# Optimization experiments

Hardware: AMD Instinct MI355X
Metric: run time of the kernel (lower is better)

## Reference

```python
import jax, jax.numpy as jnp
import numpy as np

N_NODES = 50000
N_EDGES = 800000
D = 64
H = 128


def setup_inputs() -> dict:
    key = jax.random.key(0)
    ks = jax.random.split(key, 8)
    s = 0.05
    return {
        "nodes": jax.random.normal(ks[0], (N_NODES, D), jnp.float32),
        "edges": jax.random.normal(ks[1], (N_EDGES, D), jnp.float32),
        "We1": jax.random.normal(ks[2], (3 * D, H), jnp.float32) * s,
        "be1": jnp.zeros((H,), jnp.float32),
        "We2": jax.random.normal(ks[3], (H, D), jnp.float32) * s,
        "be2": jnp.zeros((D,), jnp.float32),
        "Wn1": jax.random.normal(ks[4], (2 * D, H), jnp.float32) * s,
        "bn1": jnp.zeros((H,), jnp.float32),
        "Wn2": jax.random.normal(ks[5], (H, D), jnp.float32) * s,
        "bn2": jnp.zeros((D,), jnp.float32),
        "senders": jax.random.randint(ks[6], (N_EDGES,), 0, N_NODES, jnp.int32),
        "receivers": jax.random.randint(ks[7], (N_EDGES,), 0, N_NODES, jnp.int32),
    }


def reference(nodes, edges, We1, be1, We2, be2, Wn1, bn1, Wn2, bn2, senders, receivers):
    # EdgeBlock(use_globals=False): concat[edge, receiver_node, sender_node] -> MLP
    edge_in = jnp.concatenate([edges, nodes[receivers], nodes[senders]], axis=-1)  # [E, 3D]
    h = jax.nn.relu(edge_in @ We1 + be1)
    new_edges = h @ We2 + be2  # [E, D]

    # NodeBlock(use_sent_edges=False, use_globals=False):
    # aggregate received edges via segment_sum, concat with node feats -> MLP
    agg = jax.ops.segment_sum(new_edges, receivers, num_segments=nodes.shape[0])  # [N, D]
    node_in = jnp.concatenate([agg, nodes], axis=-1)  # [N, 2D]
    h2 = jax.nn.relu(node_in @ Wn1 + bn1)
    new_nodes = h2 @ Wn2 + bn2  # [N, D]
    return new_nodes
```

## Files before the change

kernel.cpp:

```cpp
#include <hip/hip_runtime.h>

#define NN 50000
#define NE 800000

typedef __attribute__((ext_vector_type(8))) short bf16x8;
typedef __attribute__((ext_vector_type(8))) unsigned short us8;
typedef __attribute__((ext_vector_type(4))) unsigned short us4;
typedef __attribute__((ext_vector_type(4))) float f32x4;

#define MFMA16 __builtin_amdgcn_mfma_f32_16x16x32_bf16

__device__ __forceinline__ unsigned short f2b(float f) {
    union { float f; unsigned int u; } x; x.f = f;
    unsigned int r = x.u + 0x7FFFu + ((x.u >> 16) & 1u);
    return (unsigned short)(r >> 16);
}

__device__ __forceinline__ void atomic_pk_add_bf16(unsigned short* addr, unsigned int pk) {
    asm volatile("global_atomic_pk_add_bf16 %0, %1, off" :: "v"(addr), "v"(pk) : "memory");
}

__global__ __launch_bounds__(256) void prep_kernel(
    const float* __restrict__ nodes,
    const float* __restrict__ We1, const float* __restrict__ We2,
    const float* __restrict__ Wn1, const float* __restrict__ Wn2,
    unsigned short* __restrict__ nodes_bf,
    unsigned short* __restrict__ We1T, unsigned short* __restrict__ We2T,
    unsigned short* __restrict__ Wn1T, unsigned short* __restrict__ Wn2T)
{
    const int b = blockIdx.x, t = threadIdx.x;
    if (b < 400) {
        const float4* src = (const float4*)nodes;
        for (int i = b * 256 + t; i < NN * 16; i += 400 * 256) {
            float4 v = src[i];
            us4 o; o[0] = f2b(v.x); o[1] = f2b(v.y); o[2] = f2b(v.z); o[3] = f2b(v.w);
            *(us4*)&nodes_bf[(size_t)i * 4] = o;
        }
    } else {
        const int base = (b - 400) * 256 + t;
        for (int idx = base; idx < 57344; idx += 16 * 256) {
            if (idx < 24576) {
                int n = idx / 192, k = idx % 192;
                We1T[idx] = f2b(We1[k * 128 + n]);
            } else if (idx < 32768) {
                int j = idx - 24576; int n = j / 128, k = j % 128;
                We2T[j] = f2b(We2[k * 64 + n]);
            } else if (idx < 49152) {
                int j = idx - 32768; int n = j / 128, k = j % 128;
                Wn1T[j] = f2b(Wn1[k * 128 + n]);
            } else {
                int j = idx - 49152; int n = j / 128, k = j % 128;
                Wn2T[j] = f2b(Wn2[k * 64 + n]);
            }
        }
    }
}

__global__ __launch_bounds__(256, 6) void edge_kernel(
    const unsigned short* __restrict__ nodes_bf, const float* __restrict__ edges,
    const unsigned short* __restrict__ We1T, const float* __restrict__ be1,
    const unsigned short* __restrict__ We2T, const float* __restrict__ be2,
    const int* __restrict__ senders, const int* __restrict__ receivers,
    unsigned short* __restrict__ agg_bf)
{
    __shared__ __align__(16) unsigned short xs[64 * 200];
    __shared__ int ridx[64];
    __shared__ int sidx[64];

    const int t = threadIdx.x;
    const int e0 = blockIdx.x * 64;
    const int w = t >> 6, l = t & 63, lc = l & 15, lq = l >> 4;

    if (t < 64) {
        ridx[t] = receivers[e0 + t];
        sidx[t] = senders[e0 + t];
    }

    bf16x8 wA0[6], wA1[6], wB[4];
    #pragma unroll
    for (int c = 0; c < 6; ++c) {
        wA0[c] = *(const bf16x8*)&We1T[(w * 32 + lc) * 192 + c * 32 + lq * 8];
        wA1[c] = *(const bf16x8*)&We1T[(w * 32 + 16 + lc) * 192 + c * 32 + lq * 8];
    }
    #pragma unroll
    for (int c = 0; c < 4; ++c)
        wB[c] = *(const bf16x8*)&We2T[(w * 16 + lc) * 128 + c * 32 + lq * 8];
    const float b1x = be1[w * 32 + lc];
    const float b1y = be1[w * 32 + 16 + lc];
    const float bias2 = be2[w * 16 + lc];

    __syncthreads();

    #pragma unroll
    for (int i = 0; i < 4; ++i) {
        int idx = t + 256 * i;
        int m = idx >> 4, q = idx & 15;
        float4 v = *(const float4*)&edges[((size_t)(e0 + m)) * 64 + q * 4];
        us4 o; o[0] = f2b(v.x); o[1] = f2b(v.y); o[2] = f2b(v.z); o[3] = f2b(v.w);
        *(us4*)&xs[m * 200 + q * 4] = o;
    }
    #pragma unroll
    for (int i = 0; i < 2; ++i) {
        int idx = t + 256 * i;
        int m = idx >> 3, q = idx & 7;
        us8 v = *(const us8*)&nodes_bf[(size_t)ridx[m] * 64 + q * 8];
        *(us8*)&xs[m * 200 + 64 + q * 8] = v;
    }
    #pragma unroll
    for (int i = 0; i < 2; ++i) {
        int idx = t + 256 * i;
        int m = idx >> 3, q = idx & 7;
        us8 v = *(const us8*)&nodes_bf[(size_t)sidx[m] * 64 + q * 8];
        *(us8*)&xs[m * 200 + 128 + q * 8] = v;
    }
    __syncthreads();

    f32x4 acc[4][2];
    #pragma unroll
    for (int mt = 0; mt < 4; ++mt) { acc[mt][0] = (f32x4)0.f; acc[mt][1] = (f32x4)0.f; }
    #pragma unroll
    for (int c = 0; c < 6; ++c) {
        #pragma unroll
        for (int mt = 0; mt < 4; ++mt) {
            bf16x8 a = *(const bf16x8*)&xs[(mt * 16 + lc) * 200 + c * 32 + lq * 8];
            acc[mt][0] = MFMA16(a, wA0[c], acc[mt][0], 0, 0, 0);
            acc[mt][1] = MFMA16(a, wA1[c], acc[mt][1], 0, 0, 0);
        }
    }
    __syncthreads();

    #pragma unroll
    for (int nt = 0; nt < 2; ++nt) {
        int col = w * 32 + nt * 16 + lc;
        float bias = nt ? b1y : b1x;
        #pragma unroll
        for (int mt = 0; mt < 4; ++mt) {
            #pragma unroll
            for (int r = 0; r < 4; ++r) {
                int row = mt * 16 + lq * 4 + r;
                float v = fmaxf(acc[mt][nt][r] + bias, 0.f);
                xs[row * 136 + col] = f2b(v);
            }
        }
    }
    __syncthreads();

    f32x4 acc2[4];
    #pragma unroll
    for (int mt = 0; mt < 4; ++mt) acc2[mt] = (f32x4)0.f;
    #pragma unroll
    for (int c = 0; c < 4; ++c) {
        #pragma unroll
        for (int mt = 0; mt < 4; ++mt) {
            bf16x8 a = *(const bf16x8*)&xs[(mt * 16 + lc) * 136 + c * 32 + lq * 8];
            acc2[mt] = MFMA16(a, wB[c], acc2[mt], 0, 0, 0);
        }
    }
    __syncthreads();

    float* fs = (float*)xs;
    {
        const int col = w * 16 + lc;
        #pragma unroll
        for (int mt = 0; mt < 4; ++mt) {
            #pragma unroll
            for (int r = 0; r < 4; ++r) {
                int row = mt * 16 + lq * 4 + r;
                fs[row * 68 + col] = acc2[mt][r] + bias2;
            }
        }
    }
    __syncthreads();

    #pragma unroll
    for (int i = 0; i < 8; ++i) {
        int p = t + 256 * i;
        int row = p >> 5, cp = p & 31;
        float2 v = *(const float2*)&fs[row * 68 + cp * 2];
        unsigned int pk = (unsigned int)f2b(v.x) | ((unsigned int)f2b(v.y) << 16);
        atomic_pk_add_bf16(&agg_bf[(size_t)ridx[row] * 64 + cp * 2], pk);
    }
}

__global__ __launch_bounds__(256, 6) void node_kernel(
    const unsigned short* __restrict__ nodes_bf, const unsigned short* __restrict__ agg_bf,
    const unsigned short* __restrict__ Wn1T, const float* __restrict__ bn1,
    const unsigned short* __restrict__ Wn2T, const float* __restrict__ bn2,
    float* __restrict__ out)
{
    __shared__ __align__(16) unsigned short xs[64 * 136];

    const int t = threadIdx.x;
    const int n0 = blockIdx.x * 64;
    const int w = t >> 6, l = t & 63, lc = l & 15, lq = l >> 4;

    bf16x8 wA0[4], wA1[4], wB[4];
    #pragma unroll
    for (int c = 0; c < 4; ++c) {
        wA0[c] = *(const bf16x8*)&Wn1T[(w * 32 + lc) * 128 + c * 32 + lq * 8];
        wA1[c] = *(const bf16x8*)&Wn1T[(w * 32 + 16 + lc) * 128 + c * 32 + lq * 8];
        wB[c]  = *(const bf16x8*)&Wn2T[(w * 16 + lc) * 128 + c * 32 + lq * 8];
    }
    const float b1x = bn1[w * 32 + lc];
    const float b1y = bn1[w * 32 + 16 + lc];
    const float bias2 = bn2[w * 16 + lc];

    #pragma unroll
    for (int i = 0; i < 2; ++i) {
        int idx = t + 256 * i;
        int m = idx >> 3, q = idx & 7;
        int n = n0 + m;
        us8 v = {0, 0, 0, 0, 0, 0, 0, 0};
        if (n < NN) v = *(const us8*)&agg_bf[(size_t)n * 64 + q * 8];
        *(us8*)&xs[m * 136 + q * 8] = v;
    }
    #pragma unroll
    for (int i = 0; i < 2; ++i) {
        int idx = t + 256 * i;
        int m = idx >> 3, q = idx & 7;
        int n = n0 + m;
        us8 v = {0, 0, 0, 0, 0, 0, 0, 0};
        if (n < NN) v = *(const us8*)&nodes_bf[(size_t)n * 64 + q * 8];
        *(us8*)&xs[m * 136 + 64 + q * 8] = v;
    }
    __syncthreads();

    f32x4 acc[4][2];
    #pragma unroll
    for (int mt = 0; mt < 4; ++mt) { acc[mt][0] = (f32x4)0.f; acc[mt][1] = (f32x4)0.f; }
    #pragma unroll
    for (int c = 0; c < 4; ++c) {
        #pragma unroll
        for (int mt = 0; mt < 4; ++mt) {
            bf16x8 a = *(const bf16x8*)&xs[(mt * 16 + lc) * 136 + c * 32 + lq * 8];
            acc[mt][0] = MFMA16(a, wA0[c], acc[mt][0], 0, 0, 0);
            acc[mt][1] = MFMA16(a, wA1[c], acc[mt][1], 0, 0, 0);
        }
    }
    __syncthreads();

    #pragma unroll
    for (int nt = 0; nt < 2; ++nt) {
        int col = w * 32 + nt * 16 + lc;
        float bias = nt ? b1y : b1x;
        #pragma unroll
        for (int mt = 0; mt < 4; ++mt) {
            #pragma unroll
            for (int r = 0; r < 4; ++r) {
                int row = mt * 16 + lq * 4 + r;
                float v = fmaxf(acc[mt][nt][r] + bias, 0.f);
                xs[row * 136 + col] = f2b(v);
            }
        }
    }
    __syncthreads();

    f32x4 acc2[4];
    #pragma unroll
    for (int mt = 0; mt < 4; ++mt) acc2[mt] = (f32x4)0.f;
    #pragma unroll
    for (int c = 0; c < 4; ++c) {
        #pragma unroll
        for (int mt = 0; mt < 4; ++mt) {
            bf16x8 a = *(const bf16x8*)&xs[(mt * 16 + lc) * 136 + c * 32 + lq * 8];
            acc2[mt] = MFMA16(a, wB[c], acc2[mt], 0, 0, 0);
        }
    }

    const int col = w * 16 + lc;
    #pragma unroll
    for (int mt = 0; mt < 4; ++mt) {
        #pragma unroll
        for (int r = 0; r < 4; ++r) {
            int row = mt * 16 + lq * 4 + r;
            int n = n0 + row;
            if (n < NN) out[(size_t)n * 64 + col] = acc2[mt][r] + bias2;
        }
    }
}

extern "C" void kernel_launch(void* const* d_in, const int* in_sizes, int n_in,
                              void* d_out, int out_size, void* d_ws, size_t ws_size,
                              hipStream_t stream) {
    const float* nodes = (const float*)d_in[0];
    const float* edges = (const float*)d_in[1];
    const float* We1   = (const float*)d_in[2];
    const float* be1   = (const float*)d_in[3];
    const float* We2   = (const float*)d_in[4];
    const float* be2   = (const float*)d_in[5];
    const float* Wn1   = (const float*)d_in[6];
    const float* bn1   = (const float*)d_in[7];
    const float* Wn2   = (const float*)d_in[8];
    const float* bn2   = (const float*)d_in[9];
    const int* senders   = (const int*)d_in[10];
    const int* receivers = (const int*)d_in[11];
    float* out = (float*)d_out;

    char* ws = (char*)d_ws;
    unsigned short* agg_bf = (unsigned short*)ws;
    unsigned short* nodes_bf = (unsigned short*)(ws + 12800000);
    unsigned short* We1T = (unsigned short*)(ws + 19200000);
    unsigned short* We2T = (unsigned short*)(ws + 19249152);
    unsigned short* Wn1T = (unsigned short*)(ws + 19265536);
    unsigned short* Wn2T = (unsigned short*)(ws + 19298304);

    hipMemsetAsync(agg_bf, 0, (size_t)NN * 64 * sizeof(unsigned short), stream);
    prep_kernel<<<416, 256, 0, stream>>>(nodes, We1, We2, Wn1, Wn2,
                                         nodes_bf, We1T, We2T, Wn1T, Wn2T);
    edge_kernel<<<NE / 64, 256, 0, stream>>>(nodes_bf, edges, We1T, be1, We2T, be2,
                                             senders, receivers, agg_bf);
    node_kernel<<<(NN + 63) / 64, 256, 0, stream>>>(nodes_bf, agg_bf, Wn1T, bn1, Wn2T, bn2, out);
}
```

Before: 508.4 us.

## Sort edges by receiver and reduce runs in-block before scattering to aggregates

Adds a counting-sort pipeline (histogram, three-stage scan, permutation) that groups edges by receiver. The edge kernel then processes edges in sorted order and sums each run of equal receivers in shared memory. It issues one atomic per run, or a plain store when the run is wholly inside the block. The goal is to cut the atomic traffic of the bf16 scatter. The cost is several extra small kernels and memsets, plus an indirect gather of edge rows through the permutation, which loses coalescing. Occupancy hints for edge_kernel and node_kernel are lowered from 6 to 4.

```diff
diff --git a/kernel.cpp b/kernel.cpp
--- a/kernel.cpp
+++ b/kernel.cpp
@@ -2,6 +2,8 @@
 
 #define NN 50000
 #define NE 800000
+#define NNP 50176
+#define SCANB 196
 
 typedef __attribute__((ext_vector_type(8))) short bf16x8;
 typedef __attribute__((ext_vector_type(8))) unsigned short us8;
@@ -56,24 +58,103 @@
     }
 }
 
-__global__ __launch_bounds__(256, 6) void edge_kernel(
+__global__ __launch_bounds__(256) void hist_kernel(
+    const int* __restrict__ receivers, int* __restrict__ deg)
+{
+    int e = blockIdx.x * 256 + threadIdx.x;
+    if (e < NE) atomicAdd(&deg[receivers[e]], 1);
+}
+
+__global__ __launch_bounds__(256) void scan1_kernel(
+    const int* __restrict__ deg, int* __restrict__ psum)
+{
+    __shared__ int red[256];
+    int t = threadIdx.x;
+    red[t] = deg[blockIdx.x * 256 + t];
+    __syncthreads();
+    for (int s = 128; s > 0; s >>= 1) {
+        if (t < s) red[t] += red[t + s];
+        __syncthreads();
+    }
+    if (t == 0) psum[blockIdx.x] = red[0];
+}
+
+__global__ __launch_bounds__(256) void scan2_kernel(
+    const int* __restrict__ psum, int* __restrict__ poff)
+{
+    __shared__ int a[256];
+    int t = threadIdx.x;
+    int v0 = (t < SCANB) ? psum[t] : 0;
+    a[t] = v0;
+    __syncthreads();
+    for (int off = 1; off < 256; off <<= 1) {
+        int x = a[t];
+        if (t >= off) x += a[t - off];
+        __syncthreads();
+        a[t] = x;
+        __syncthreads();
+    }
+    poff[t] = a[t] - v0;
+}
+
+__global__ __launch_bounds__(256) void scan3_kernel(
+    const int* __restrict__ deg, const int* __restrict__ poff, int* __restrict__ basep)
+{
+    __shared__ int a[256];
+    int t = threadIdx.x, i = blockIdx.x * 256 + t;
+    int v0 = deg[i];
+    a[t] = v0;
+    __syncthreads();
+    for (int off = 1; off < 256; off <<= 1) {
+        int x = a[t];
+        if (t >= off) x += a[t - off];
+        __syncthreads();
+        a[t] = x;
+        __syncthreads();
+    }
+    basep[i] = poff[blockIdx.x] + a[t] - v0;
+}
+
+__global__ __launch_bounds__(256) void perm_kernel(
+    const int* __restrict__ receivers, const int* __restrict__ senders,
+    const int* __restrict__ basep, int* __restrict__ cursor,
+    int* __restrict__ perm, int* __restrict__ rsorted, int* __restrict__ ssorted)
+{
+    int e = blockIdx.x * 256 + threadIdx.x;
+    if (e < NE) {
+        int r = receivers[e];
+        int pos = basep[r] + atomicAdd(&cursor[r], 1);
+        perm[pos] = e;
+        rsorted[pos] = r;
+        ssorted[pos] = senders[e];
+    }
+}
+
+__global__ __launch_bounds__(256, 4) void edge_kernel(
     const unsigned short* __restrict__ nodes_bf, const float* __restrict__ edges,
     const unsigned short* __restrict__ We1T, const float* __restrict__ be1,
     const unsigned short* __restrict__ We2T, const float* __restrict__ be2,
-    const int* __restrict__ senders, const int* __restrict__ receivers,
+    const int* __restrict__ perm, const int* __restrict__ rsorted,
+    const int* __restrict__ ssorted, const int* __restrict__ basep,
     unsigned short* __restrict__ agg_bf)
 {
     __shared__ __align__(16) unsigned short xs[64 * 200];
+    __shared__ int eidx[64];
     __shared__ int ridx[64];
     __shared__ int sidx[64];
+    __shared__ int runStart[65];
+    __shared__ int runRecv[64];
+    __shared__ int runFull[64];
+    __shared__ int nrunsS;
 
     const int t = threadIdx.x;
     const int e0 = blockIdx.x * 64;
     const int w = t >> 6, l = t & 63, lc = l & 15, lq = l >> 4;
 
     if (t < 64) {
-        ridx[t] = receivers[e0 + t];
-        sidx[t] = senders[e0 + t];
+        eidx[t] = perm[e0 + t];
+        ridx[t] = rsorted[e0 + t];
+        sidx[t] = ssorted[e0 + t];
     }
 
     bf16x8 wA0[6], wA1[6], wB[4];
@@ -91,11 +172,26 @@
 
     __syncthreads();
 
+    if (t < 64) {
+        int n = ridx[t];
+        bool flag = (t == 0) || (n != ridx[t - 1]);
+        unsigned long long mask = __ballot(flag);
+        int nr = __popcll(mask);
+        if (t == 0) { nrunsS = nr; runStart[nr] = 64; }
+        if (flag) {
+            int rank = __popcll(mask & ((1ULL << t) - 1ULL));
+            runStart[rank] = t;
+            runRecv[rank] = n;
+            int s = basep[n], e = basep[n + 1];
+            runFull[rank] = (s >= e0) && (e <= e0 + 64);
+        }
+    }
+
     #pragma unroll
     for (int i = 0; i < 4; ++i) {
         int idx = t + 256 * i;
         int m = idx >> 4, q = idx & 15;
-        float4 v = *(const float4*)&edges[((size_t)(e0 + m)) * 64 + q * 4];
+        float4 v = *(const float4*)&edges[(size_t)eidx[m] * 64 + q * 4];
         us4 o; o[0] = f2b(v.x); o[1] = f2b(v.y); o[2] = f2b(v.z); o[3] = f2b(v.w);
         *(us4*)&xs[m * 200 + q * 4] = o;
     }
@@ -172,17 +268,23 @@
     }
     __syncthreads();
 
-    #pragma unroll
-    for (int i = 0; i < 8; ++i) {
-        int p = t + 256 * i;
-        int row = p >> 5, cp = p & 31;
-        float2 v = *(const float2*)&fs[row * 68 + cp * 2];
-        unsigned int pk = (unsigned int)f2b(v.x) | ((unsigned int)f2b(v.y) << 16);
-        atomic_pk_add_bf16(&agg_bf[(size_t)ridx[row] * 64 + cp * 2], pk);
-    }
-}
-
-__global__ __launch_bounds__(256, 6) void node_kernel(
+    const int nr = nrunsS;
+    const int cp = t & 31;
+    for (int ri = t >> 5; ri < nr; ri += 8) {
+        int rs = runStart[ri], re = runStart[ri + 1];
+        float s0 = 0.f, s1 = 0.f;
+        for (int r = rs; r < re; ++r) {
+            float2 v = *(const float2*)&fs[r * 68 + cp * 2];
+            s0 += v.x; s1 += v.y;
+        }
+        unsigned int pk = (unsigned int)f2b(s0) | ((unsigned int)f2b(s1) << 16);
+        unsigned short* addr = &agg_bf[(size_t)runRecv[ri] * 64 + cp * 2];
+        if (runFull[ri]) *(unsigned int*)addr = pk;
+        else             atomic_pk_add_bf16(addr, pk);
+    }
+}
+
+__global__ __launch_bounds__(256, 4) void node_kernel(
     const unsigned short* __restrict__ nodes_bf, const unsigned short* __restrict__ agg_bf,
     const unsigned short* __restrict__ Wn1T, const float* __restrict__ bn1,
     const unsigned short* __restrict__ Wn2T, const float* __restrict__ bn2,
@@ -297,17 +399,33 @@
     float* out = (float*)d_out;
 
     char* ws = (char*)d_ws;
-    unsigned short* agg_bf = (unsigned short*)ws;
-    unsigned short* nodes_bf = (unsigned short*)(ws + 12800000);
-    unsigned short* We1T = (unsigned short*)(ws + 19200000);
-    unsigned short* We2T = (unsigned short*)(ws + 19249152);
-    unsigned short* Wn1T = (unsigned short*)(ws + 19265536);
-    unsigned short* Wn2T = (unsigned short*)(ws + 19298304);
-
+    unsigned short* agg_bf   = (unsigned short*)ws;
+    unsigned short* nodes_bf = (unsigned short*)(ws +  6400000);
+    unsigned short* We1T = (unsigned short*)(ws + 12800000);
+    unsigned short* We2T = (unsigned short*)(ws + 12849152);
+    unsigned short* Wn1T = (unsigned short*)(ws + 12865536);
+    unsigned short* Wn2T = (unsigned short*)(ws + 12898304);
+    int* perm    = (int*)(ws + 12914688);
+    int* rsorted = (int*)(ws + 16114688);
+    int* ssorted = (int*)(ws + 19314688);
+    int* deg     = (int*)(ws + 22514688);
+    int* basep   = (int*)(ws + 22715392);
+    int* cursor  = (int*)(ws + 22916096);
+    int* psum    = (int*)(ws + 23116096);
+    int* poff    = (int*)(ws + 23117120);
+
+    hipMemsetAsync(deg, 0, NNP * sizeof(int), stream);
+    hipMemsetAsync(cursor, 0, NN * sizeof(int), stream);
     hipMemsetAsync(agg_bf, 0, (size_t)NN * 64 * sizeof(unsigned short), stream);
     prep_kernel<<<416, 256, 0, stream>>>(nodes, We1, We2, Wn1, Wn2,
                                          nodes_bf, We1T, We2T, Wn1T, Wn2T);
+    hist_kernel<<<(NE + 255) / 256, 256, 0, stream>>>(receivers, deg);
+    scan1_kernel<<<SCANB, 256, 0, stream>>>(deg, psum);
+    scan2_kernel<<<1, 256, 0, stream>>>(psum, poff);
+    scan3_kernel<<<SCANB, 256, 0, stream>>>(deg, poff, basep);
+    perm_kernel<<<(NE + 255) / 256, 256, 0, stream>>>(receivers, senders, basep, cursor,
+                                                      perm, rsorted, ssorted);
     edge_kernel<<<NE / 64, 256, 0, stream>>>(nodes_bf, edges, We1T, be1, We2T, be2,
-                                             senders, receivers, agg_bf);
+                                             perm, rsorted, ssorted, basep, agg_bf);
     node_kernel<<<(NN + 63) / 64, 256, 0, stream>>>(nodes_bf, agg_bf, Wn1T, bn1, Wn2T, bn2, out);
 }
```

Result: faster. 494.7 us (-2.7%).
